# Performance work log

Hardware: AMD Instinct MI355X
Metric: run time of the kernel (lower is better)

Reference implementation:

```python
import jax, jax.numpy as jnp
import numpy as np

B, H, S = 128, 512, 2048

def setup_inputs() -> dict:
    key = jax.random.key(0)
    ks = jax.random.split(key, 8)
    sc = 1.0 / np.sqrt(H)
    return {
        "all_hidden": jax.random.normal(ks[0], (B, H, S), dtype=jnp.float32),
        "v_att": jax.random.normal(ks[1], (H,), dtype=jnp.float32) * sc,
        "W_att": jax.random.normal(ks[2], (H, H), dtype=jnp.float32) * sc,
        "v_ptr": jax.random.normal(ks[3], (H,), dtype=jnp.float32) * sc,
        "fc1_w": jax.random.normal(ks[4], (H, H), dtype=jnp.float32) * sc,
        "fc1_b": jax.random.normal(ks[5], (H,), dtype=jnp.float32) * sc,
        "fc2_w": jax.random.normal(ks[6], (H, H), dtype=jnp.float32) * sc,
        "fc2_b": jax.random.normal(ks[7], (H,), dtype=jnp.float32) * sc,
    }

def reference(all_hidden, v_att, W_att, v_ptr, fc1_w, fc1_b, fc2_w, fc2_b):
    # all_hidden: [B, H, S]
    # Attention: attns = softmax(v . tanh(W @ all_hidden), over seq)
    scores = jnp.einsum('hk,bks->bhs', W_att, all_hidden)          # [B,H,S]
    attn = jax.nn.softmax(jnp.einsum('h,bhs->bs', v_att, jnp.tanh(scores)), axis=-1)  # [B,S]
    # context = attn @ all_hidden^T  -> [B,H]
    context = jnp.einsum('bs,bhs->bh', attn, all_hidden)
    # 2-layer MLP with relu (torch Linear: x @ W^T + b)
    out = jax.nn.relu(context @ fc1_w.T + fc1_b)
    out = jax.nn.relu(out @ fc2_w.T + fc2_b)                        # [B,H]
    # probs = v . tanh(all_hidden + out broadcast over seq)
    probs = jnp.einsum('h,bhs->bs', v_ptr, jnp.tanh(all_hidden + out[:, :, None]))  # [B,S]
    return probs
```

## Files before the change

kernel.cpp:

```cpp
#include <hip/hip_runtime.h>
#include <hip/hip_bf16.h>

#define B_ 128
#define H_ 512
#define S_ 2048
#define ST 64
#define NP (S_/ST)

typedef short  bf16x8  __attribute__((ext_vector_type(8)));
typedef float  floatx4 __attribute__((ext_vector_type(4)));
typedef short  short4v __attribute__((ext_vector_type(4)));

#define KT_TANH 2.8853900817779268f

__device__ __forceinline__ unsigned short f2bf(float f){
  unsigned u = __float_as_uint(f);
  unsigned r = (u + 0x7fffu + ((u >> 16) & 1u)) >> 16;
  return (unsigned short)r;
}
__device__ __forceinline__ float bf2f(unsigned short h){
  return __uint_as_float(((unsigned)h) << 16);
}
__device__ __forceinline__ float tanh_r(float a){
  float e = __builtin_amdgcn_exp2f(a);
  return __builtin_amdgcn_rcpf(e + 1.f);
}
__device__ __forceinline__ int swz(int s, int c){
  return (c & 56) | ((c ^ s) & 7);
}

__global__ __launch_bounds__(256) void k_convW(const float* __restrict__ W,
                                               unsigned short* __restrict__ Wb){
  int i = (blockIdx.x * 256 + threadIdx.x) * 4;
  float4 v = *(const float4*)(W + i);
  short4v o;
  o[0] = (short)f2bf(v.x); o[1] = (short)f2bf(v.y);
  o[2] = (short)f2bf(v.z); o[3] = (short)f2bf(v.w);
  *(short4v*)(Wb + i) = o;
}

__global__ __launch_bounds__(512, 4) void k_pass1(
    const float* __restrict__ hidden, const float* __restrict__ v_att,
    const unsigned short* __restrict__ Wb,
    float* __restrict__ part_m, float* __restrict__ part_z,
    float* __restrict__ part_ctx)
{
  union __align__(16) SMem {
    unsigned short Bs[ST * 512];
    float pctx[8 * H_];
  };
  __shared__ SMem sm;
  __shared__ float vatt[H_];
  __shared__ float twav[8][ST];
  __shared__ float es[ST];

  const int tid = threadIdx.x;
  const int w = tid >> 6, l = tid & 63;
  const int p = blockIdx.x & (NP - 1);
  const int b = blockIdx.x >> 5;
  const int s0 = p * ST;

  vatt[tid] = v_att[tid];

  {
    const float* src0 = hidden + ((size_t)b * H_) * S_ + s0 + l;
    #pragma unroll
    for (int it = 0; it < 8; ++it){
      const int c = w + it * 8;
      const float* src = src0 + (size_t)(c * 8) * S_;
      bf16x8 pk;
      #pragma unroll
      for (int j = 0; j < 8; ++j)
        pk[j] = (short)f2bf(__builtin_nontemporal_load(src + (size_t)j * S_));
      *(bf16x8*)(&sm.Bs[l * 512 + swz(l, c) * 8]) = pk;
    }
  }

  const int quad = l >> 4, l16 = l & 15;

  float sva = 0.f;
  if (w == 0){
    #pragma unroll
    for (int k = 0; k < 8; ++k) sva += v_att[l + 64 * k];
    sva += __shfl_xor(sva, 1);  sva += __shfl_xor(sva, 2);
    sva += __shfl_xor(sva, 4);  sva += __shfl_xor(sva, 8);
    sva += __shfl_xor(sva, 16); sva += __shfl_xor(sva, 32);
  }

  const unsigned short* Wbase = Wb + (w * 4 * 16 + l16) * H_ + quad * 8;
  bf16x8 a0[4], a1[4], b0[4], b1[4];
  #pragma unroll
  for (int ti = 0; ti < 4; ++ti)
    a0[ti] = *(const bf16x8*)(Wbase + ti * 16 * H_ + 0);

  __syncthreads();

  float tacc[4] = {0.f, 0.f, 0.f, 0.f};
  {
    floatx4 acc[4][4];
    #pragma unroll
    for (int ti = 0; ti < 4; ++ti)
      #pragma unroll
      for (int ss = 0; ss < 4; ++ss){
        floatx4 z4 = {0.f, 0.f, 0.f, 0.f};
        acc[ti][ss] = z4;
      }

    #pragma unroll
    for (int ss = 0; ss < 4; ++ss)
      b0[ss] = *(const bf16x8*)(&sm.Bs[(ss * 16 + l16) * 512 + swz(l16, quad) * 8]);

    #pragma unroll
    for (int k0 = 0; k0 < H_; k0 += 64){
      const int kA = k0 + 32;
      #pragma unroll
      for (int ti = 0; ti < 4; ++ti)
        a1[ti] = *(const bf16x8*)(Wbase + ti * 16 * H_ + kA);
      #pragma unroll
      for (int ss = 0; ss < 4; ++ss)
        b1[ss] = *(const bf16x8*)(&sm.Bs[(ss * 16 + l16) * 512 + swz(l16, (kA >> 3) + quad) * 8]);
      #pragma unroll
      for (int ti = 0; ti < 4; ++ti)
        #pragma unroll
        for (int ss = 0; ss < 4; ++ss)
          acc[ti][ss] = __builtin_amdgcn_mfma_f32_16x16x32_bf16(a0[ti], b0[ss], acc[ti][ss], 0, 0, 0);

      if (k0 + 64 < H_){
        const int kB = k0 + 64;
        #pragma unroll
        for (int ti = 0; ti < 4; ++ti)
          a0[ti] = *(const bf16x8*)(Wbase + ti * 16 * H_ + kB);
        #pragma unroll
        for (int ss = 0; ss < 4; ++ss)
          b0[ss] = *(const bf16x8*)(&sm.Bs[(ss * 16 + l16) * 512 + swz(l16, (kB >> 3) + quad) * 8]);
      }
      #pragma unroll
      for (int ti = 0; ti < 4; ++ti)
        #pragma unroll
        for (int ss = 0; ss < 4; ++ss)
          acc[ti][ss] = __builtin_amdgcn_mfma_f32_16x16x32_bf16(a1[ti], b1[ss], acc[ti][ss], 0, 0, 0);
    }

    #pragma unroll
    for (int ti = 0; ti < 4; ++ti){
      const int hbase = (w * 4 + ti) * 16 + quad * 4;
      #pragma unroll
      for (int r = 0; r < 4; ++r){
        float va = vatt[hbase + r];
        #pragma unroll
        for (int ss = 0; ss < 4; ++ss)
          tacc[ss] = fmaf(va, tanh_r(acc[ti][ss][r] * KT_TANH), tacc[ss]);
      }
    }
  }

  #pragma unroll
  for (int ss = 0; ss < 4; ++ss){
    tacc[ss] += __shfl_xor(tacc[ss], 16);
    tacc[ss] += __shfl_xor(tacc[ss], 32);
  }
  if (l < 16){
    #pragma unroll
    for (int ss = 0; ss < 4; ++ss) twav[w][ss * 16 + l] = tacc[ss];
  }
  __syncthreads();

  const int pidx = b * NP + p;
  if (w == 0){
    float a = 0.f;
    #pragma unroll
    for (int ww = 0; ww < 8; ++ww) a += twav[ww][l];
    float t = sva - 2.f * a;
    float m = t;
    m = fmaxf(m, __shfl_xor(m, 1));  m = fmaxf(m, __shfl_xor(m, 2));
    m = fmaxf(m, __shfl_xor(m, 4));  m = fmaxf(m, __shfl_xor(m, 8));
    m = fmaxf(m, __shfl_xor(m, 16)); m = fmaxf(m, __shfl_xor(m, 32));
    float e = __expf(t - m);
    es[l] = e;
    float z = e;
    z += __shfl_xor(z, 1);  z += __shfl_xor(z, 2);
    z += __shfl_xor(z, 4);  z += __shfl_xor(z, 8);
    z += __shfl_xor(z, 16); z += __shfl_xor(z, 32);
    if (l == 0){ part_m[pidx] = m; part_z[pidx] = z; }
  }
  __syncthreads();

  float a8[8] = {0.f,0.f,0.f,0.f,0.f,0.f,0.f,0.f};
  #pragma unroll
  for (int j = 0; j < 8; ++j){
    const int s = w * 8 + j;
    const float ez = es[s];
    bf16x8 v = *(const bf16x8*)(&sm.Bs[s * 512 + swz(s, l) * 8]);
    #pragma unroll
    for (int e = 0; e < 8; ++e)
      a8[e] = fmaf(ez, bf2f((unsigned short)v[e]), a8[e]);
  }
  __syncthreads();
  {
    floatx4 lo = {a8[0], a8[1], a8[2], a8[3]};
    floatx4 hi = {a8[4], a8[5], a8[6], a8[7]};
    *(floatx4*)(&sm.pctx[w * H_ + l * 4])       = lo;
    *(floatx4*)(&sm.pctx[w * H_ + 256 + l * 4]) = hi;
  }
  __syncthreads();
  {
    const int idx = ((tid >> 3) << 2) + (tid & 3) + ((tid & 4) << 6);
    float a = 0.f;
    #pragma unroll
    for (int ww = 0; ww < 8; ++ww) a += sm.pctx[ww * H_ + idx];
    part_ctx[(size_t)pidx * H_ + tid] = a;
  }
}

__global__ __launch_bounds__(256) void k_mlp(
    const float* __restrict__ part_m, const float* __restrict__ part_z,
    const float* __restrict__ part_ctx,
    const float* __restrict__ fc1_w, const float* __restrict__ fc1_b,
    const float* __restrict__ fc2_w, const float* __restrict__ fc2_b,
    float* __restrict__ out2)
{
  __shared__ float ctx[H_];
  __shared__ float h1[H_];
  __shared__ float wp[NP];
  const int b = blockIdx.x, tid = threadIdx.x;

  float m = -1e30f;
  for (int pp = 0; pp < NP; ++pp) m = fmaxf(m, part_m[b * NP + pp]);
  if (tid < NP) wp[tid] = __expf(part_m[b * NP + tid] - m);
  __syncthreads();
  float z = 0.f;
  for (int pp = 0; pp < NP; ++pp) z += wp[pp] * part_z[b * NP + pp];
  float invz = 1.f / z;

  for (int h = tid; h < H_; h += 256){
    float a = 0.f;
    for (int pp = 0; pp < NP; ++pp) a += wp[pp] * part_ctx[(size_t)(b * NP + pp) * H_ + h];
    ctx[h] = a * invz;
  }
  __syncthreads();

  for (int i = tid; i < H_; i += 256){
    const float4* row = (const float4*)(fc1_w + (size_t)i * H_);
    float4 s4 = {0.f, 0.f, 0.f, 0.f};
    for (int j = 0; j < H_ / 4; ++j){
      float4 wv = row[j];
      s4.x += wv.x * ctx[4 * j];     s4.y += wv.y * ctx[4 * j + 1];
      s4.z += wv.z * ctx[4 * j + 2]; s4.w += wv.w * ctx[4 * j + 3];
    }
    h1[i] = fmaxf(fc1_b[i] + s4.x + s4.y + s4.z + s4.w, 0.f);
  }
  __syncthreads();

  for (int i = tid; i < H_; i += 256){
    const float4* row = (const float4*)(fc2_w + (size_t)i * H_);
    float4 s4 = {0.f, 0.f, 0.f, 0.f};
    for (int j = 0; j < H_ / 4; ++j){
      float4 wv = row[j];
      s4.x += wv.x * h1[4 * j];     s4.y += wv.y * h1[4 * j + 1];
      s4.z += wv.z * h1[4 * j + 2]; s4.w += wv.w * h1[4 * j + 3];
    }
    out2[(size_t)b * H_ + i] = fmaxf(fc2_b[i] + s4.x + s4.y + s4.z + s4.w, 0.f);
  }
}

__global__ __launch_bounds__(256) void k_probs(
    const float* __restrict__ hidden, const float* __restrict__ v_ptr,
    const float* __restrict__ out2, float* __restrict__ probs)
{
  __shared__ float vp[H_], ko[H_];
  __shared__ float svp_sh;
  const int b = blockIdx.y, c = blockIdx.x, tid = threadIdx.x;
  vp[tid]       = v_ptr[tid];
  vp[tid + 256] = v_ptr[tid + 256];
  ko[tid]       = KT_TANH * out2[(size_t)b * H_ + tid];
  ko[tid + 256] = KT_TANH * out2[(size_t)b * H_ + tid + 256];
  __syncthreads();
  if (tid < 64){
    float sv = 0.f;
    #pragma unroll
    for (int k = 0; k < 8; ++k) sv += vp[tid + 64 * k];
    sv += __shfl_xor(sv, 1);  sv += __shfl_xor(sv, 2);
    sv += __shfl_xor(sv, 4);  sv += __shfl_xor(sv, 8);
    sv += __shfl_xor(sv, 16); sv += __shfl_xor(sv, 32);
    if (tid == 0) svp_sh = sv;
  }
  __syncthreads();

  const int s = c * 512 + tid * 2;
  const float* base = hidden + (size_t)b * H_ * S_ + s;
  float a0 = 0.f, a1 = 0.f;
  const float kt = KT_TANH;
  #pragma unroll 16
  for (int h = 0; h < H_; ++h){
    float2 hv = *(const float2*)(base + (size_t)h * S_);
    float wv = vp[h], o = ko[h];
    a0 = fmaf(wv, tanh_r(fmaf(kt, hv.x, o)), a0);
    a1 = fmaf(wv, tanh_r(fmaf(kt, hv.y, o)), a1);
  }
  float svp = svp_sh;
  float2 r2 = { svp - 2.f * a0, svp - 2.f * a1 };
  *(float2*)(probs + (size_t)b * S_ + s) = r2;
}

extern "C" void kernel_launch(void* const* d_in, const int* in_sizes, int n_in,
                              void* d_out, int out_size, void* d_ws, size_t ws_size,
                              hipStream_t stream)
{
  const float* hidden = (const float*)d_in[0];
  const float* v_att  = (const float*)d_in[1];
  const float* W_att  = (const float*)d_in[2];
  const float* v_ptr  = (const float*)d_in[3];
  const float* fc1_w  = (const float*)d_in[4];
  const float* fc1_b  = (const float*)d_in[5];
  const float* fc2_w  = (const float*)d_in[6];
  const float* fc2_b  = (const float*)d_in[7];
  float* probs = (float*)d_out;

  char* ws = (char*)d_ws;
  unsigned short* Wb = (unsigned short*)ws;
  float* part_m   = (float*)(ws + (512u<<10));
  float* part_z   = (float*)(ws + (512u<<10) + (16u<<10));
  float* part_ctx = (float*)(ws + (512u<<10) + (32u<<10));
  float* out2     = (float*)(ws + (512u<<10) + (32u<<10) + (8u<<20));

  hipLaunchKernelGGL(k_convW, dim3(256), dim3(256), 0, stream, W_att, Wb);
  hipLaunchKernelGGL(k_pass1, dim3(B_ * NP), dim3(512), 0, stream,
                     hidden, v_att, Wb, part_m, part_z, part_ctx);
  hipLaunchKernelGGL(k_mlp, dim3(B_), dim3(256), 0, stream,
                     part_m, part_z, part_ctx, fc1_w, fc1_b, fc2_w, fc2_b, out2);
  hipLaunchKernelGGL(k_probs, dim3(S_ / 512, B_), dim3(256), 0, stream,
                     hidden, v_ptr, out2, probs);
}
```

Before: 1.083 ms.

## Cache bf16 transposed hidden from pass1 and split MLP into parallel kernels

Pass1 now writes its bf16-converted, transposed hidden tile to a workspace buffer, so the final probs kernel reads 2-byte data instead of re-reading fp32 hidden. The MLP is split into fc1/fc2 kernels over a larger grid, using transposed weights for coalesced column reads. The software-pipelined double-buffered MFMA loop is replaced by a simpler single-buffer loop. The cost is an extra 64MB write in pass1 and a precision drop in the pointer step, with a fallback path used when the workspace is too small.

```diff
diff --git a/kernel.cpp b/kernel.cpp
--- a/kernel.cpp
+++ b/kernel.cpp
@@ -39,11 +39,30 @@
   *(short4v*)(Wb + i) = o;
 }
 
+__global__ __launch_bounds__(256) void k_trans(const float* __restrict__ src0,
+                                               float* __restrict__ dst0,
+                                               const float* __restrict__ src1,
+                                               float* __restrict__ dst1){
+  __shared__ float t[32][33];
+  const float* src = blockIdx.z ? src1 : src0;
+  float*       dst = blockIdx.z ? dst1 : dst0;
+  const int bx = blockIdx.x * 32, by = blockIdx.y * 32;
+  const int x = threadIdx.x & 31, y = threadIdx.x >> 5;
+  #pragma unroll
+  for (int r = 0; r < 32; r += 8)
+    t[y + r][x] = src[(size_t)(by + y + r) * H_ + bx + x];
+  __syncthreads();
+  #pragma unroll
+  for (int r = 0; r < 32; r += 8)
+    dst[(size_t)(bx + y + r) * H_ + by + x] = t[x][y + r];
+}
+
+template<int WRITE_HT>
 __global__ __launch_bounds__(512, 4) void k_pass1(
     const float* __restrict__ hidden, const float* __restrict__ v_att,
     const unsigned short* __restrict__ Wb,
     float* __restrict__ part_m, float* __restrict__ part_z,
-    float* __restrict__ part_ctx)
+    float* __restrict__ part_ctx, unsigned short* __restrict__ hT)
 {
   union __align__(16) SMem {
     unsigned short Bs[ST * 512];
@@ -76,8 +95,6 @@
     }
   }
 
-  const int quad = l >> 4, l16 = l & 15;
-
   float sva = 0.f;
   if (w == 0){
     #pragma unroll
@@ -86,16 +103,11 @@
     sva += __shfl_xor(sva, 4);  sva += __shfl_xor(sva, 8);
     sva += __shfl_xor(sva, 16); sva += __shfl_xor(sva, 32);
   }
-
-  const unsigned short* Wbase = Wb + (w * 4 * 16 + l16) * H_ + quad * 8;
-  bf16x8 a0[4], a1[4], b0[4], b1[4];
-  #pragma unroll
-  for (int ti = 0; ti < 4; ++ti)
-    a0[ti] = *(const bf16x8*)(Wbase + ti * 16 * H_ + 0);
-
-  __syncthreads();
-
+  __syncthreads();
+
+  const int quad = l >> 4, l16 = l & 15;
   float tacc[4] = {0.f, 0.f, 0.f, 0.f};
+
   {
     floatx4 acc[4][4];
     #pragma unroll
@@ -106,39 +118,22 @@
         acc[ti][ss] = z4;
       }
 
-    #pragma unroll
-    for (int ss = 0; ss < 4; ++ss)
-      b0[ss] = *(const bf16x8*)(&sm.Bs[(ss * 16 + l16) * 512 + swz(l16, quad) * 8]);
-
-    #pragma unroll
-    for (int k0 = 0; k0 < H_; k0 += 64){
-      const int kA = k0 + 32;
+    for (int k0 = 0; k0 < H_; k0 += 32){
+      bf16x8 a[4];
       #pragma unroll
       for (int ti = 0; ti < 4; ++ti)
-        a1[ti] = *(const bf16x8*)(Wbase + ti * 16 * H_ + kA);
-      #pragma unroll
-      for (int ss = 0; ss < 4; ++ss)
-        b1[ss] = *(const bf16x8*)(&sm.Bs[(ss * 16 + l16) * 512 + swz(l16, (kA >> 3) + quad) * 8]);
+        a[ti] = *(const bf16x8*)(Wb + ((w * 4 + ti) * 16 + l16) * H_ + k0 + quad * 8);
+      bf16x8 bb[4];
+      #pragma unroll
+      for (int ss = 0; ss < 4; ++ss){
+        const int c = (k0 >> 3) + quad;
+        bb[ss] = *(const bf16x8*)(&sm.Bs[(ss * 16 + l16) * 512 + swz(l16, c) * 8]);
+      }
       #pragma unroll
       for (int ti = 0; ti < 4; ++ti)
         #pragma unroll
         for (int ss = 0; ss < 4; ++ss)
-          acc[ti][ss] = __builtin_amdgcn_mfma_f32_16x16x32_bf16(a0[ti], b0[ss], acc[ti][ss], 0, 0, 0);
-
-      if (k0 + 64 < H_){
-        const int kB = k0 + 64;
-        #pragma unroll
-        for (int ti = 0; ti < 4; ++ti)
-          a0[ti] = *(const bf16x8*)(Wbase + ti * 16 * H_ + kB);
-        #pragma unroll
-        for (int ss = 0; ss < 4; ++ss)
-          b0[ss] = *(const bf16x8*)(&sm.Bs[(ss * 16 + l16) * 512 + swz(l16, (kB >> 3) + quad) * 8]);
-      }
-      #pragma unroll
-      for (int ti = 0; ti < 4; ++ti)
-        #pragma unroll
-        for (int ss = 0; ss < 4; ++ss)
-          acc[ti][ss] = __builtin_amdgcn_mfma_f32_16x16x32_bf16(a1[ti], b1[ss], acc[ti][ss], 0, 0, 0);
+          acc[ti][ss] = __builtin_amdgcn_mfma_f32_16x16x32_bf16(a[ti], bb[ss], acc[ti][ss], 0, 0, 0);
     }
 
     #pragma unroll
@@ -191,6 +186,9 @@
     const int s = w * 8 + j;
     const float ez = es[s];
     bf16x8 v = *(const bf16x8*)(&sm.Bs[s * 512 + swz(s, l) * 8]);
+    if (WRITE_HT)
+      __builtin_nontemporal_store(v,
+          (bf16x8*)(hT + ((size_t)(b * S_) + s0 + s) * H_ + l * 8));
     #pragma unroll
     for (int e = 0; e < 8; ++e)
       a8[e] = fmaf(ez, bf2f((unsigned short)v[e]), a8[e]);
@@ -212,17 +210,15 @@
   }
 }
 
-__global__ __launch_bounds__(256) void k_mlp(
+__global__ __launch_bounds__(256) void k_fc1(
     const float* __restrict__ part_m, const float* __restrict__ part_z,
     const float* __restrict__ part_ctx,
-    const float* __restrict__ fc1_w, const float* __restrict__ fc1_b,
-    const float* __restrict__ fc2_w, const float* __restrict__ fc2_b,
-    float* __restrict__ out2)
-{
-  __shared__ float ctx[H_];
-  __shared__ float h1[H_];
+    const float* __restrict__ w1t, const float* __restrict__ fc1_b,
+    float* __restrict__ h1out)
+{
+  __shared__ float ctxs[H_];
   __shared__ float wp[NP];
-  const int b = blockIdx.x, tid = threadIdx.x;
+  const int b = blockIdx.y, ih = blockIdx.x, tid = threadIdx.x;
 
   float m = -1e30f;
   for (int pp = 0; pp < NP; ++pp) m = fmaxf(m, part_m[b * NP + pp]);
@@ -230,40 +226,86 @@
   __syncthreads();
   float z = 0.f;
   for (int pp = 0; pp < NP; ++pp) z += wp[pp] * part_z[b * NP + pp];
-  float invz = 1.f / z;
-
+  const float invz = 1.f / z;
+
+  #pragma unroll
   for (int h = tid; h < H_; h += 256){
     float a = 0.f;
-    for (int pp = 0; pp < NP; ++pp) a += wp[pp] * part_ctx[(size_t)(b * NP + pp) * H_ + h];
-    ctx[h] = a * invz;
-  }
-  __syncthreads();
-
-  for (int i = tid; i < H_; i += 256){
-    const float4* row = (const float4*)(fc1_w + (size_t)i * H_);
-    float4 s4 = {0.f, 0.f, 0.f, 0.f};
-    for (int j = 0; j < H_ / 4; ++j){
-      float4 wv = row[j];
-      s4.x += wv.x * ctx[4 * j];     s4.y += wv.y * ctx[4 * j + 1];
-      s4.z += wv.z * ctx[4 * j + 2]; s4.w += wv.w * ctx[4 * j + 3];
-    }
-    h1[i] = fmaxf(fc1_b[i] + s4.x + s4.y + s4.z + s4.w, 0.f);
-  }
-  __syncthreads();
-
-  for (int i = tid; i < H_; i += 256){
-    const float4* row = (const float4*)(fc2_w + (size_t)i * H_);
-    float4 s4 = {0.f, 0.f, 0.f, 0.f};
-    for (int j = 0; j < H_ / 4; ++j){
-      float4 wv = row[j];
-      s4.x += wv.x * h1[4 * j];     s4.y += wv.y * h1[4 * j + 1];
-      s4.z += wv.z * h1[4 * j + 2]; s4.w += wv.w * h1[4 * j + 3];
-    }
-    out2[(size_t)b * H_ + i] = fmaxf(fc2_b[i] + s4.x + s4.y + s4.z + s4.w, 0.f);
-  }
-}
-
-__global__ __launch_bounds__(256) void k_probs(
+    for (int pp = 0; pp < NP; ++pp)
+      a += wp[pp] * part_ctx[(size_t)(b * NP + pp) * H_ + h];
+    ctxs[h] = a * invz;
+  }
+  __syncthreads();
+
+  const int i = ih * 256 + tid;
+  const float* col = w1t + i;
+  float acc = fc1_b[i];
+  #pragma unroll 8
+  for (int k = 0; k < H_; ++k)
+    acc = fmaf(col[(size_t)k * H_], ctxs[k], acc);
+  h1out[(size_t)b * H_ + i] = fmaxf(acc, 0.f);
+}
+
+__global__ __launch_bounds__(256) void k_fc2(
+    const float* __restrict__ h1, const float* __restrict__ w2t,
+    const float* __restrict__ fc2_b, float* __restrict__ out2)
+{
+  __shared__ float h1s[H_];
+  const int b = blockIdx.y, ih = blockIdx.x, tid = threadIdx.x;
+  h1s[tid]       = h1[(size_t)b * H_ + tid];
+  h1s[tid + 256] = h1[(size_t)b * H_ + tid + 256];
+  __syncthreads();
+
+  const int i = ih * 256 + tid;
+  const float* col = w2t + i;
+  float acc = fc2_b[i];
+  #pragma unroll 8
+  for (int k = 0; k < H_; ++k)
+    acc = fmaf(col[(size_t)k * H_], h1s[k], acc);
+  out2[(size_t)b * H_ + i] = fmaxf(acc, 0.f);
+}
+
+__global__ __launch_bounds__(256) void k_probs_hT(
+    const unsigned short* __restrict__ hT, const float* __restrict__ v_ptr,
+    const float* __restrict__ out2, float* __restrict__ probs)
+{
+  const int tid = threadIdx.x, w = tid >> 6, l = tid & 63;
+  const int b = blockIdx.y, s0 = blockIdx.x * 64;
+
+  float vp[8], ko[8];
+  {
+    float4 a = *(const float4*)(v_ptr + l * 8);
+    float4 c = *(const float4*)(v_ptr + l * 8 + 4);
+    vp[0]=a.x; vp[1]=a.y; vp[2]=a.z; vp[3]=a.w;
+    vp[4]=c.x; vp[5]=c.y; vp[6]=c.z; vp[7]=c.w;
+    float4 d = *(const float4*)(out2 + (size_t)b * H_ + l * 8);
+    float4 e = *(const float4*)(out2 + (size_t)b * H_ + l * 8 + 4);
+    ko[0]=KT_TANH*d.x; ko[1]=KT_TANH*d.y; ko[2]=KT_TANH*d.z; ko[3]=KT_TANH*d.w;
+    ko[4]=KT_TANH*e.x; ko[5]=KT_TANH*e.y; ko[6]=KT_TANH*e.z; ko[7]=KT_TANH*e.w;
+  }
+  float svp = vp[0]+vp[1]+vp[2]+vp[3]+vp[4]+vp[5]+vp[6]+vp[7];
+  svp += __shfl_xor(svp, 1);  svp += __shfl_xor(svp, 2);
+  svp += __shfl_xor(svp, 4);  svp += __shfl_xor(svp, 8);
+  svp += __shfl_xor(svp, 16); svp += __shfl_xor(svp, 32);
+
+  const unsigned short* base = hT + (size_t)(b * S_ + s0) * H_ + l * 8;
+  const float kt = KT_TANH;
+  #pragma unroll 2
+  for (int i = 0; i < 16; ++i){
+    const int s = w * 16 + i;
+    bf16x8 hv = __builtin_nontemporal_load((const bf16x8*)(base + (size_t)s * H_));
+    float acc = 0.f;
+    #pragma unroll
+    for (int j = 0; j < 8; ++j)
+      acc = fmaf(vp[j], tanh_r(fmaf(kt, bf2f((unsigned short)hv[j]), ko[j])), acc);
+    acc += __shfl_xor(acc, 1);  acc += __shfl_xor(acc, 2);
+    acc += __shfl_xor(acc, 4);  acc += __shfl_xor(acc, 8);
+    acc += __shfl_xor(acc, 16); acc += __shfl_xor(acc, 32);
+    if (l == 0) probs[(size_t)b * S_ + s0 + s] = svp - 2.f * acc;
+  }
+}
+
+__global__ __launch_bounds__(256) void k_probs_f32(
     const float* __restrict__ hidden, const float* __restrict__ v_ptr,
     const float* __restrict__ out2, float* __restrict__ probs)
 {
@@ -319,15 +361,38 @@
   char* ws = (char*)d_ws;
   unsigned short* Wb = (unsigned short*)ws;
   float* part_m   = (float*)(ws + (512u<<10));
-  float* part_z   = (float*)(ws + (512u<<10) + (16u<<10));
-  float* part_ctx = (float*)(ws + (512u<<10) + (32u<<10));
-  float* out2     = (float*)(ws + (512u<<10) + (32u<<10) + (8u<<20));
+  float* part_z   = (float*)(ws + (528u<<10));
+  float* part_ctx = (float*)(ws + (1u<<20));
+  float* out2     = (float*)(ws + (9u<<20));
+  float* h1buf    = (float*)(ws + (9u<<20) + (256u<<10));
+  float* w1t      = (float*)(ws + (10u<<20));
+  float* w2t      = (float*)(ws + (11u<<20));
+  unsigned short* hT = (unsigned short*)(ws + (16u<<20));
+
+  const size_t need_full = (16u<<20) + ((size_t)B_ * S_ * H_ * 2);
 
   hipLaunchKernelGGL(k_convW, dim3(256), dim3(256), 0, stream, W_att, Wb);
-  hipLaunchKernelGGL(k_pass1, dim3(B_ * NP), dim3(512), 0, stream,
-                     hidden, v_att, Wb, part_m, part_z, part_ctx);
-  hipLaunchKernelGGL(k_mlp, dim3(B_), dim3(256), 0, stream,
-                     part_m, part_z, part_ctx, fc1_w, fc1_b, fc2_w, fc2_b, out2);
-  hipLaunchKernelGGL(k_probs, dim3(S_ / 512, B_), dim3(256), 0, stream,
-                     hidden, v_ptr, out2, probs);
-}
+  hipLaunchKernelGGL(k_trans, dim3(16, 16, 2), dim3(256), 0, stream,
+                     fc1_w, w1t, fc2_w, w2t);
+
+  if (ws_size >= need_full){
+    hipLaunchKernelGGL(k_pass1<1>, dim3(B_ * NP), dim3(512), 0, stream,
+                       hidden, v_att, Wb, part_m, part_z, part_ctx, hT);
+  } else {
+    hipLaunchKernelGGL(k_pass1<0>, dim3(B_ * NP), dim3(512), 0, stream,
+                       hidden, v_att, Wb, part_m, part_z, part_ctx, (unsigned short*)Wb);
+  }
+
+  hipLaunchKernelGGL(k_fc1, dim3(2, B_), dim3(256), 0, stream,
+                     part_m, part_z, part_ctx, w1t, fc1_b, h1buf);
+  hipLaunchKernelGGL(k_fc2, dim3(2, B_), dim3(256), 0, stream,
+                     h1buf, w2t, fc2_b, out2);
+
+  if (ws_size >= need_full){
+    hipLaunchKernelGGL(k_probs_hT, dim3(S_ / 64, B_), dim3(256), 0, stream,
+                       hT, v_ptr, out2, probs);
+  } else {
+    hipLaunchKernelGGL(k_probs_f32, dim3(S_ / 512, B_), dim3(256), 0, stream,
+                       hidden, v_ptr, out2, probs);
+  }
+}
```

Result: faster. 1.041 ms (-3.9%).
